# Optimization experiments

Hardware: AMD Instinct MI355X
Metric: run time of the kernel (lower is better)

The kernel has to match this reference:

```python
import jax, jax.numpy as jnp
import numpy as np

B, D = 4096, 512
N_PROTO = 1000          # prototype tasks
CLS_PER_TASK = 10       # indices*10 block size in original code
N_CLASSES = N_PROTO * CLS_PER_TASK
NUM_TEST = 10


def setup_inputs() -> dict:
    key = jax.random.key(0)
    k1, k2, k3 = jax.random.split(key, 3)
    img = jax.random.normal(k1, (B, D), dtype=jnp.float32)
    # image encoder output is L2-normalized and detached in the original
    image_features = img / jnp.linalg.norm(img, axis=-1, keepdims=True)
    ima_proto = jax.random.normal(k2, (N_PROTO, D), dtype=jnp.float32)
    ima_proto = ima_proto / jnp.linalg.norm(ima_proto, axis=-1, keepdims=True)
    text_features_raw = jax.random.normal(k3, (N_CLASSES, D), dtype=jnp.float32)
    logit_scale = jnp.asarray(np.log(1.0 / 0.07), dtype=jnp.float32)  # CLIP init
    return {
        "image_features": image_features,
        "ima_proto": ima_proto,
        "text_features_raw": text_features_raw,
        "logit_scale": logit_scale,
        "num_test": NUM_TEST,
    }


def reference(image_features, ima_proto, text_features_raw, logit_scale, num_test):
    n_proto = ima_proto.shape[0]
    n_classes = text_features_raw.shape[0]
    b = image_features.shape[0]
    k = min(int(num_test), n_proto)

    # probability = image_features @ ima_proto.t(); topk indices
    probability = image_features @ ima_proto.T                      # [B, n_proto]
    _, indices = jax.lax.top_k(probability, k)                      # [B, k]

    # text_features normalized, logit = image_features @ text_features.t()
    text_features = text_features_raw / jnp.linalg.norm(
        text_features_raw, axis=-1, keepdims=True)
    logit = image_features @ text_features.T                        # [B, n_classes]

    # vectorized form of the double loop:
    #   logits[j][idx*10 : idx*10+10] = logit[j][idx*10 : idx*10+10]
    sel = jnp.zeros((b, n_proto), dtype=logit.dtype)
    sel = sel.at[jnp.arange(b)[:, None], indices].set(1.0)          # [B, n_proto]
    block_of_class = jnp.arange(n_classes) // CLS_PER_TASK          # [n_classes]
    mask = sel[:, block_of_class]                                   # [B, n_classes]

    logits = jnp.exp(logit_scale) * (logit * mask)
    return logits
```

## Files before the change

kernel.cpp:

```cpp
#include <hip/hip_runtime.h>
#include <cfloat>
#include <math.h>

#define B_ROWS   4096
#define DIM      512
#define NPROTO   1000
#define NCLASSES 10000
#define KSEL     10
#define KCAND    16
#define CAP      256
#define PROB_LD  1024

#define PROB_BYTES 16777216u
#define OUT_BYTES  163840000u
#define ZHI_N4     ((OUT_BYTES - PROB_BYTES) / 16)
#define ZQ1        5000000u
#define ZS1        0u
#define ZQ2        (ZHI_N4 - ZQ1)
#define ZS2        ZQ1

#define GBM 64
#define GBN 128
#define GBK 32
#define ALD 40

typedef short s16x8 __attribute__((ext_vector_type(8)));
typedef float f32x4 __attribute__((ext_vector_type(4)));

static __device__ __forceinline__ unsigned short f2bf(float f) {
  unsigned int x = __float_as_uint(f);
  return (unsigned short)((x + 0x7fffu + ((x >> 16) & 1u)) >> 16);
}

static __device__ __forceinline__ s16x8 cvt8(float4 a, float4 b) {
  s16x8 r;
  r[0]=f2bf(a.x); r[1]=f2bf(a.y); r[2]=f2bf(a.z); r[3]=f2bf(a.w);
  r[4]=f2bf(b.x); r[5]=f2bf(b.y); r[6]=f2bf(b.z); r[7]=f2bf(b.w);
  return r;
}

static __device__ __forceinline__ void zero_share(
    f32x4* __restrict__ zhi, unsigned start, unsigned count,
    unsigned gth, unsigned nthreads)
{
  const f32x4 z4 = (f32x4)0.f;
  for (unsigned i = start + gth; i < start + count; i += nthreads)
    __builtin_nontemporal_store(z4, zhi + i);
}

__global__ __launch_bounds__(256) void k_gemm(
    const float* __restrict__ img, const float* __restrict__ proto,
    float* __restrict__ prob, f32x4* __restrict__ zhi,
    int* __restrict__ counts)
{
  __shared__ short Al[GBM * ALD];
  __shared__ short Bl[GBN * ALD];

  const int tid  = threadIdx.x;
  const int lane = tid & 63, wave = tid >> 6;
  const int wr = wave >> 1, wc = wave & 1;
  const int row0 = blockIdx.x * GBM;
  const int col0 = blockIdx.y * GBN;
  const unsigned gth = (blockIdx.y * gridDim.x + blockIdx.x) * 256 + tid;

  const int sr = tid >> 2;
  const int sc = (tid & 3) * 8;

  int pa = col0 + sr;      if (pa > NPROTO - 1) pa = NPROTO - 1;
  int pb = col0 + 64 + sr; if (pb > NPROTO - 1) pb = NPROTO - 1;
  const float* gA  = img   + (size_t)(row0 + sr) * DIM + sc;
  const float* gB0 = proto + (size_t)pa * DIM + sc;
  const float* gB1 = proto + (size_t)pb * DIM + sc;

  float4 ra0  = *(const float4*)(gA);      float4 ra1  = *(const float4*)(gA + 4);
  float4 rb00 = *(const float4*)(gB0);     float4 rb01 = *(const float4*)(gB0 + 4);
  float4 rb10 = *(const float4*)(gB1);     float4 rb11 = *(const float4*)(gB1 + 4);

  f32x4 acc[2][4];
#pragma unroll
  for (int m = 0; m < 2; ++m)
#pragma unroll
    for (int n = 0; n < 4; ++n) acc[m][n] = (f32x4)0.f;

  const int kg = lane >> 4;
  const int fr = lane & 15;

  for (int kt = 0; kt < DIM / GBK; ++kt) {
    *(s16x8*)&Al[sr * ALD + sc]        = cvt8(ra0, ra1);
    *(s16x8*)&Bl[sr * ALD + sc]        = cvt8(rb00, rb01);
    *(s16x8*)&Bl[(64 + sr) * ALD + sc] = cvt8(rb10, rb11);
    __syncthreads();

    if (kt + 1 < DIM / GBK) {
      const int k0 = (kt + 1) * GBK;
      ra0  = *(const float4*)(gA + k0);   ra1  = *(const float4*)(gA + k0 + 4);
      rb00 = *(const float4*)(gB0 + k0);  rb01 = *(const float4*)(gB0 + k0 + 4);
      rb10 = *(const float4*)(gB1 + k0);  rb11 = *(const float4*)(gB1 + k0 + 4);
    }

    s16x8 af[2], bf[4];
#pragma unroll
    for (int m = 0; m < 2; ++m)
      af[m] = *(const s16x8*)&Al[(wr * 32 + m * 16 + fr) * ALD + kg * 8];
#pragma unroll
    for (int n = 0; n < 4; ++n)
      bf[n] = *(const s16x8*)&Bl[(wc * 64 + n * 16 + fr) * ALD + kg * 8];
#pragma unroll
    for (int m = 0; m < 2; ++m)
#pragma unroll
      for (int n = 0; n < 4; ++n)
        acc[m][n] = __builtin_amdgcn_mfma_f32_16x16x32_bf16(
            af[m], bf[n], acc[m][n], 0, 0, 0);
    __syncthreads();
  }

#pragma unroll
  for (int m = 0; m < 2; ++m)
#pragma unroll
    for (int n = 0; n < 4; ++n) {
      const int r = row0 + wr * 32 + m * 16 + (lane >> 4) * 4;
      const int c = col0 + wc * 64 + n * 16 + fr;
#pragma unroll
      for (int reg = 0; reg < 4; ++reg)
        prob[(size_t)(r + reg) * PROB_LD + c] = acc[m][n][reg];
    }

  if (blockIdx.x == 0 && blockIdx.y == 0)
    for (int i = tid; i < NPROTO; i += 256) counts[i] = 0;

  zero_share(zhi, ZS1, ZQ1, gth, 512 * 256);
}

__global__ __launch_bounds__(256) void k_select(
    float* __restrict__ prob, const float* __restrict__ img,
    const float* __restrict__ proto, int* __restrict__ counts,
    int* __restrict__ buckets, f32x4* __restrict__ zhi)
{
  __shared__ float srow[4][PROB_LD];
  const int tid  = threadIdx.x;
  const int wave = tid >> 6, lane = tid & 63;
  const int row  = blockIdx.x * 4 + wave;

  const float* p = prob + (size_t)row * PROB_LD;
#pragma unroll
  for (int i = 0; i < PROB_LD / 64; ++i) {
    const int j = lane + i * 64;
    srow[wave][j] = (j < NPROTO) ? p[j] : -FLT_MAX;
  }

  int ci[KCAND];
  for (int kk = 0; kk < KCAND; ++kk) {
    float bv = -FLT_MAX;
    int   bi = 0x7fffffff;
#pragma unroll
    for (int i = 0; i < PROB_LD / 64; ++i) {
      const int j = lane + i * 64;
      float v = srow[wave][j];
      if (v > bv || (v == bv && j < bi)) { bv = v; bi = j; }
    }
#pragma unroll
    for (int off = 32; off; off >>= 1) {
      float ov = __shfl_down(bv, off);
      int   oi = __shfl_down(bi, off);
      if (ov > bv || (ov == bv && oi < bi)) { bv = ov; bi = oi; }
    }
    bi = __shfl(bi, 0);
    ci[kk] = bi;
    srow[wave][bi] = -FLT_MAX;
  }

  {
    const f32x4 z4 = (f32x4)0.f;
    f32x4* prow = reinterpret_cast<f32x4*>(prob + (size_t)row * PROB_LD);
#pragma unroll
    for (int i = 0; i < 4; ++i)
      __builtin_nontemporal_store(z4, prow + lane + i * 64);
  }

  const float4* a4 = reinterpret_cast<const float4*>(img + (size_t)row * DIM);
  const float4 a0 = a4[lane], a1 = a4[64 + lane];
  float dv[KCAND];
#pragma unroll
  for (int j = 0; j < KCAND; ++j) {
    const float4* p4 = reinterpret_cast<const float4*>(proto + (size_t)ci[j] * DIM);
    const float4 b0 = p4[lane], b1 = p4[64 + lane];
    float s = 0.f;
    s = fmaf(a0.x, b0.x, s); s = fmaf(a0.y, b0.y, s);
    s = fmaf(a0.z, b0.z, s); s = fmaf(a0.w, b0.w, s);
    s = fmaf(a1.x, b1.x, s); s = fmaf(a1.y, b1.y, s);
    s = fmaf(a1.z, b1.z, s); s = fmaf(a1.w, b1.w, s);
#pragma unroll
    for (int off = 32; off; off >>= 1) s += __shfl_xor(s, off);
    dv[j] = s;
  }

  unsigned picked = 0;
  for (int kk = 0; kk < KSEL; ++kk) {
    float bv = -FLT_MAX;
    int   bj = 0;
#pragma unroll
    for (int j = 0; j < KCAND; ++j)
      if (!((picked >> j) & 1u) && dv[j] > bv) { bv = dv[j]; bj = j; }
    picked |= 1u << bj;
    if (lane == kk) {
      const int pp  = ci[bj];
      const int pos = atomicAdd(&counts[pp], 1);
      if (pos < CAP) buckets[pp * CAP + pos] = row;
    }
  }

  zero_share(zhi, ZS2, ZQ2, blockIdx.x * 256 + tid, 1024 * 256);
}

__global__ __launch_bounds__(256) void k_compute(
    const float* __restrict__ img, const float* __restrict__ text,
    const int* __restrict__ counts, const int* __restrict__ buckets,
    const float* __restrict__ logit_scale, float* __restrict__ out)
{
  __shared__ float stext[KSEL * DIM];
  __shared__ float sfac[KSEL];

  const int p    = blockIdx.x;
  const int tid  = threadIdx.x;
  const int wave = tid >> 6, lane = tid & 63;

  {
    const float4* src = reinterpret_cast<const float4*>(text + (size_t)p * KSEL * DIM);
    float4* dst = reinterpret_cast<float4*>(stext);
#pragma unroll
    for (int i = 0; i < 5; ++i) dst[tid + i * 256] = src[tid + i * 256];
  }
  __syncthreads();

  const float scale = expf(logit_scale[0]);
#pragma unroll
  for (int j = wave; j < KSEL; j += 4) {
    const float4* t4 = reinterpret_cast<const float4*>(stext + j * DIM);
    float4 v0 = t4[lane], v1 = t4[64 + lane];
    float s = 0.f;
    s = fmaf(v0.x, v0.x, s); s = fmaf(v0.y, v0.y, s);
    s = fmaf(v0.z, v0.z, s); s = fmaf(v0.w, v0.w, s);
    s = fmaf(v1.x, v1.x, s); s = fmaf(v1.y, v1.y, s);
    s = fmaf(v1.z, v1.z, s); s = fmaf(v1.w, v1.w, s);
#pragma unroll
    for (int off = 32; off; off >>= 1) s += __shfl_down(s, off);
    if (lane == 0) sfac[j] = scale / sqrtf(s);
  }
  __syncthreads();

  {
    float4* st4 = reinterpret_cast<float4*>(stext);
#pragma unroll
    for (int i = 0; i < 5; ++i) {
      const int idx = tid + i * 256;
      const float f = sfac[idx >> 7];
      float4 v = st4[idx];
      v.x *= f; v.y *= f; v.z *= f; v.w *= f;
      st4[idx] = v;
    }
  }
  __syncthreads();

  const int n = min(counts[p], CAP);
  const float4* st4 = reinterpret_cast<const float4*>(stext);

  for (int i = wave; i < n; i += 4) {
    const int row = buckets[p * CAP + i];
    const float4* a4 = reinterpret_cast<const float4*>(img + (size_t)row * DIM);
    const float4 a0 = a4[lane], a1 = a4[64 + lane];

    float acc[KSEL];
#pragma unroll
    for (int j = 0; j < KSEL; ++j) {
      const float4 b0 = st4[j * 128 + lane];
      const float4 b1 = st4[j * 128 + 64 + lane];
      float s = 0.f;
      s = fmaf(a0.x, b0.x, s); s = fmaf(a0.y, b0.y, s);
      s = fmaf(a0.z, b0.z, s); s = fmaf(a0.w, b0.w, s);
      s = fmaf(a1.x, b1.x, s); s = fmaf(a1.y, b1.y, s);
      s = fmaf(a1.z, b1.z, s); s = fmaf(a1.w, b1.w, s);
      acc[j] = s;
    }
#pragma unroll
    for (int j = 0; j < KSEL; ++j) {
#pragma unroll
      for (int off = 32; off; off >>= 1)
        acc[j] += __shfl_xor(acc[j], off);
    }
    float v = acc[0];
#pragma unroll
    for (int j = 1; j < KSEL; ++j) if (lane == j) v = acc[j];
    if (lane < KSEL)
      out[(size_t)row * NCLASSES + p * KSEL + lane] = v;
  }
}

extern "C" void kernel_launch(void* const* d_in, const int* in_sizes, int n_in,
                              void* d_out, int out_size, void* d_ws, size_t ws_size,
                              hipStream_t stream) {
  const float* img    = (const float*)d_in[0];
  const float* proto  = (const float*)d_in[1];
  const float* text   = (const float*)d_in[2];
  const float* lscale = (const float*)d_in[3];

  float*  prob = (float*)d_out;
  f32x4*  zhi  = (f32x4*)((char*)d_out + PROB_BYTES);
  float*  out  = (float*)d_out;

  int* counts  = (int*)d_ws;
  int* buckets = (int*)((char*)d_ws + 4096);

  k_gemm<<<dim3(B_ROWS / GBM, 1024 / GBN), 256, 0, stream>>>(
      img, proto, prob, zhi, counts);
  k_select<<<B_ROWS / 4, 256, 0, stream>>>(prob, img, proto, counts, buckets, zhi);
  k_compute<<<NPROTO, 256, 0, stream>>>(img, text, counts, buckets, lscale, out);
}
```

Baseline: 122.5 us.

## Store prototype scores as fp16, shrink candidates, prefetch rows, defer text scaling

The intermediate probability matrix is now stored as fp16 instead of fp32, halving its scratch footprint in the output buffer and the bytes read back in the selection kernel. The candidate count for exact fp32 re-ranking drops from 16 to 12, and the zero-fill split between kernels is rebalanced. In the compute kernel the next image row is prefetched into registers, and the per-class normalisation scale is applied at the output store instead of in a separate shared-memory pass. Fp16 scores and fewer candidates increase the risk of choosing a different top-10 set when scores are close.

```diff
diff --git a/kernel.cpp b/kernel.cpp
--- a/kernel.cpp
+++ b/kernel.cpp
@@ -7,14 +7,14 @@
 #define NPROTO   1000
 #define NCLASSES 10000
 #define KSEL     10
-#define KCAND    16
+#define KCAND    12
 #define CAP      256
 #define PROB_LD  1024
 
-#define PROB_BYTES 16777216u
+#define PROB_BYTES 8388608u
 #define OUT_BYTES  163840000u
 #define ZHI_N4     ((OUT_BYTES - PROB_BYTES) / 16)
-#define ZQ1        5000000u
+#define ZQ1        6000000u
 #define ZS1        0u
 #define ZQ2        (ZHI_N4 - ZQ1)
 #define ZS2        ZQ1
@@ -31,12 +31,19 @@
   unsigned int x = __float_as_uint(f);
   return (unsigned short)((x + 0x7fffu + ((x >> 16) & 1u)) >> 16);
 }
-
 static __device__ __forceinline__ s16x8 cvt8(float4 a, float4 b) {
   s16x8 r;
   r[0]=f2bf(a.x); r[1]=f2bf(a.y); r[2]=f2bf(a.z); r[3]=f2bf(a.w);
   r[4]=f2bf(b.x); r[5]=f2bf(b.y); r[6]=f2bf(b.z); r[7]=f2bf(b.w);
   return r;
+}
+static __device__ __forceinline__ unsigned short f2h(float f) {
+  _Float16 h = (_Float16)f;
+  return __builtin_bit_cast(unsigned short, h);
+}
+static __device__ __forceinline__ float h2f(unsigned short u) {
+  _Float16 h = __builtin_bit_cast(_Float16, u);
+  return (float)h;
 }
 
 static __device__ __forceinline__ void zero_share(
@@ -50,7 +57,7 @@
 
 __global__ __launch_bounds__(256) void k_gemm(
     const float* __restrict__ img, const float* __restrict__ proto,
-    float* __restrict__ prob, f32x4* __restrict__ zhi,
+    unsigned short* __restrict__ prob, f32x4* __restrict__ zhi,
     int* __restrict__ counts)
 {
   __shared__ short Al[GBM * ALD];
@@ -122,7 +129,7 @@
       const int c = col0 + wc * 64 + n * 16 + fr;
 #pragma unroll
       for (int reg = 0; reg < 4; ++reg)
-        prob[(size_t)(r + reg) * PROB_LD + c] = acc[m][n][reg];
+        prob[(size_t)(r + reg) * PROB_LD + c] = f2h(acc[m][n][reg]);
     }
 
   if (blockIdx.x == 0 && blockIdx.y == 0)
@@ -132,7 +139,7 @@
 }
 
 __global__ __launch_bounds__(256) void k_select(
-    float* __restrict__ prob, const float* __restrict__ img,
+    unsigned short* __restrict__ prob, const float* __restrict__ img,
     const float* __restrict__ proto, int* __restrict__ counts,
     int* __restrict__ buckets, f32x4* __restrict__ zhi)
 {
@@ -141,11 +148,17 @@
   const int wave = tid >> 6, lane = tid & 63;
   const int row  = blockIdx.x * 4 + wave;
 
-  const float* p = prob + (size_t)row * PROB_LD;
-#pragma unroll
-  for (int i = 0; i < PROB_LD / 64; ++i) {
-    const int j = lane + i * 64;
-    srow[wave][j] = (j < NPROTO) ? p[j] : -FLT_MAX;
+  {
+    const unsigned* pu = reinterpret_cast<const unsigned*>(
+        prob + (size_t)row * PROB_LD);
+#pragma unroll
+    for (int i = 0; i < 8; ++i) {
+      const int idx = lane + i * 64;
+      const unsigned u = pu[idx];
+      const int c0 = idx * 2;
+      srow[wave][c0]     = (c0     < NPROTO) ? h2f((unsigned short)(u & 0xffff)) : -FLT_MAX;
+      srow[wave][c0 + 1] = (c0 + 1 < NPROTO) ? h2f((unsigned short)(u >> 16))    : -FLT_MAX;
+    }
   }
 
   int ci[KCAND];
@@ -172,9 +185,8 @@
   {
     const f32x4 z4 = (f32x4)0.f;
     f32x4* prow = reinterpret_cast<f32x4*>(prob + (size_t)row * PROB_LD);
-#pragma unroll
-    for (int i = 0; i < 4; ++i)
-      __builtin_nontemporal_store(z4, prow + lane + i * 64);
+    __builtin_nontemporal_store(z4, prow + lane);
+    __builtin_nontemporal_store(z4, prow + 64 + lane);
   }
 
   const float4* a4 = reinterpret_cast<const float4*>(img + (size_t)row * DIM);
@@ -248,26 +260,25 @@
   }
   __syncthreads();
 
-  {
-    float4* st4 = reinterpret_cast<float4*>(stext);
-#pragma unroll
-    for (int i = 0; i < 5; ++i) {
-      const int idx = tid + i * 256;
-      const float f = sfac[idx >> 7];
-      float4 v = st4[idx];
-      v.x *= f; v.y *= f; v.z *= f; v.w *= f;
-      st4[idx] = v;
-    }
-  }
-  __syncthreads();
-
   const int n = min(counts[p], CAP);
   const float4* st4 = reinterpret_cast<const float4*>(stext);
+  const int* bkt = buckets + p * CAP;
+
+  int row = -1, nrow;
+  float4 a0, a1, na0, na1;
+  if (wave < n) {
+    row = bkt[wave];
+    const float4* a4 = reinterpret_cast<const float4*>(img + (size_t)row * DIM);
+    a0 = a4[lane]; a1 = a4[64 + lane];
+  }
 
   for (int i = wave; i < n; i += 4) {
-    const int row = buckets[p * CAP + i];
-    const float4* a4 = reinterpret_cast<const float4*>(img + (size_t)row * DIM);
-    const float4 a0 = a4[lane], a1 = a4[64 + lane];
+    const int inext = i + 4;
+    if (inext < n) {
+      nrow = bkt[inext];
+      const float4* a4 = reinterpret_cast<const float4*>(img + (size_t)nrow * DIM);
+      na0 = a4[lane]; na1 = a4[64 + lane];
+    }
 
     float acc[KSEL];
 #pragma unroll
@@ -291,7 +302,9 @@
 #pragma unroll
     for (int j = 1; j < KSEL; ++j) if (lane == j) v = acc[j];
     if (lane < KSEL)
-      out[(size_t)row * NCLASSES + p * KSEL + lane] = v;
+      out[(size_t)row * NCLASSES + p * KSEL + lane] = v * sfac[lane];
+
+    row = nrow; a0 = na0; a1 = na1;
   }
 }
 
@@ -303,7 +316,7 @@
   const float* text   = (const float*)d_in[2];
   const float* lscale = (const float*)d_in[3];
 
-  float*  prob = (float*)d_out;
+  unsigned short* prob = (unsigned short*)d_out;
   f32x4*  zhi  = (f32x4*)((char*)d_out + PROB_BYTES);
   float*  out  = (float*)d_out;
 
```

New measurement: 110.9 us. -9.5%, faster.
